# Kernel optimization log

Measured on AMD Instinct MI355X. Metric: run time of the kernel, lower is better.

The kernel has to match this reference:

```python
import jax, jax.numpy as jnp
import numpy as np

# ---- constants mirroring the torch module ----
OSAMP = 8            # temporal oversampling factor
MAX_ITER = 10        # forward solver iterations (LBFGS replaced by fixed GD)
NEG_SHIFT = 2 * OSAMP
OTP = 5              # baseline frames subtracted from ctc/aif
C_SHARP = 500.0      # sharpness constant C=500 in fermi_ir_func
LR = 0.1             # fixed step size for the deterministic forward solve


def interp_linear_1d(x, size):
    # interp_linear_1D: linear upsampling along last (time) axis
    return jax.image.resize(x, x.shape[:-1] + (size,), method='linear')


def fermi_ir(eta, t_os):
    # eta: [B,3,H,W] = (amplitude A, decay rate k, delay t0); t_os: [Tos]
    tsh = t_os - t_os[NEG_SHIFT]                    # negative time shift
    A = eta[:, 0][..., None]                        # [B,H,W,1]
    k = eta[:, 1][..., None]
    t0 = eta[:, 2][..., None]
    step = jax.nn.sigmoid(C_SHARP * tsh)            # sharp causal onset (C=500)
    return A * jax.nn.sigmoid(k * (t0 - tsh)) * step  # [B,H,W,Tos]


def convolve(aif, ir):
    # linear convolution along time via FFT; output aligned with neg_shift offset
    Tos = ir.shape[-1]
    n = 2 * Tos
    Fa = jnp.fft.rfft(aif, n=n, axis=-1)            # [B,1,1,n/2+1]
    Fi = jnp.fft.rfft(ir, n=n, axis=-1)             # [B,H,W,n/2+1]
    full = jnp.fft.irfft(Fa * Fi, n=n, axis=-1)
    return jax.lax.dynamic_slice_in_dim(full, NEG_SHIFT, Tos, axis=-1)


def make_objective(ctc, aif, time, eta_prior, lambda_reg):
    # preprocessing from FermiDataConsLBFGS.forward
    aif = aif - aif[..., :OTP].mean(-1, keepdims=True)
    ctc = ctc - ctc[..., :OTP].mean(-1, keepdims=True)
    Tos = OSAMP * ctc.shape[-1]
    aif_os = interp_linear_1d(aif, Tos)
    ctc_os = interp_linear_1d(ctc, Tos)
    t_os = interp_linear_1d(time, Tos)
    ctc_dc = ctc_os[..., ::OSAMP]                   # [B,H,W,T]
    C_nn = (eta_prior ** 2).sum(axis=(0, 2, 3), keepdims=True)  # [1,3,1,1]
    C_dc = (ctc_dc ** 2).sum()
    sp_lam = jax.nn.softplus(lambda_reg).squeeze()

    def F_obj(eta):  # FermiDConsObj.__call__ (OD disabled: indx_dc = all frames)
        ir = fermi_ir(eta, t_os)
        ctc_est = convolve(aif_os, ir)[..., ::OSAMP] / OSAMP
        dc = ((ctc_dc - ctc_est) ** 2 / C_dc).sum()
        reg = sp_lam * (((eta - eta_prior) ** 2) / C_nn).sum()
        pos = (jax.nn.relu(-eta) ** 2).sum()
        return dc + reg + pos
    return F_obj


def setup_inputs():
    key = jax.random.key(0)
    k1, k2, k3, k4 = jax.random.split(key, 4)
    B, H, W, T = 1, 128, 128, 64
    ctc = jax.random.normal(k1, (B, H, W, T), jnp.float32) * 0.1
    aif = jax.random.uniform(k2, (B, 1, 1, T), jnp.float32)
    time = jnp.arange(T, dtype=jnp.float32)
    seg = jnp.ones((B, H, W), jnp.int32)
    eta_nn = jax.random.uniform(k3, (B, 3, H, W), jnp.float32)
    lambda_reg = jax.random.normal(k4, (1,), jnp.float32)
    return {"ctc": ctc, "aif": aif, "time": time, "seg": seg,
            "eta_nn": eta_nn, "lambda_reg": lambda_reg}


def reference(ctc, aif, time, seg, eta_nn, lambda_reg):
    # seg only affects the (disabled) outlier-detection path
    F_obj = make_objective(ctc, aif, time, eta_nn, lambda_reg)
    gradF = jax.grad(F_obj)

    def step(eta, _):
        return eta - LR * gradF(eta), None

    eta_pi, _ = jax.lax.scan(step, eta_nn, None, length=MAX_ITER)
    return eta_pi
```

## Files before the change

kernel.cpp:

```cpp
#include <hip/hip_runtime.h>
#include <math.h>

#define T_IN 64
#define NPIX 16384
#define MAX_ITER 10
#define NSLOT 43
#define MAGIC 0x13579BDFu

typedef _Float16 half8_t __attribute__((ext_vector_type(8)));
typedef __fp16   fp16x2  __attribute__((ext_vector_type(2)));
typedef float    f32x4   __attribute__((ext_vector_type(4)));
typedef int      i32x4   __attribute__((ext_vector_type(4)));

union H8 { half8_t v; fp16x2 h2[4]; i32x4 i4; };

__device__ __forceinline__ float rcp_fast(float x) { return __builtin_amdgcn_rcpf(x); }

__global__ __launch_bounds__(256, 1) void k_all(
        const float* __restrict__ ctc,  const float* __restrict__ aif,
        const float* __restrict__ timev,const float* __restrict__ lam,
        const float* __restrict__ eta,  unsigned int* __restrict__ flags,
        f32x4* __restrict__ partials,   float* __restrict__ out) {
    __shared__ i32x4 Bs[NSLOT * 64];
    __shared__ float tshs[512];
    __shared__ float aifos[512];
    __shared__ float a_s[64], t_s[64];
    __shared__ f32x4 red[4];

    const int tid  = threadIdx.x;
    const int lane = tid & 63;
    const int wid  = tid >> 6;
    const int q = lane >> 4, n = lane & 15;
    const int pixbase = blockIdx.x * 64 + wid * 16;
    const int mypix   = pixbase + n;

    if (tid < 64) { a_s[tid] = aif[tid]; t_s[tid] = timev[tid]; }
    float A  = eta[mypix];
    float K  = eta[NPIX + mypix];
    float T0 = eta[2*NPIX + mypix];
    const float pA = A, pK = K, pT = T0;
    __syncthreads();
    {
        float m5a = 0.2f * (a_s[0]+a_s[1]+a_s[2]+a_s[3]+a_s[4]);
        float t16;
        {
            float xx = 1.5625f; int i0 = (int)xx; float f = xx - (float)i0;
            t16 = t_s[i0]*(1.0f-f) + t_s[i0+1]*f;
        }
        #pragma unroll
        for (int rep = 0; rep < 2; ++rep) {
            int i = tid + 256*rep;
            float x = ((float)i - 3.5f) * 0.125f;
            float ao, to;
            if (x <= 0.0f)       { ao = a_s[0]  - m5a; to = t_s[0];  }
            else if (x >= 63.0f) { ao = a_s[63] - m5a; to = t_s[63]; }
            else {
                int i0 = (int)x; float f = x - (float)i0;
                ao = (a_s[i0]-m5a)*(1.0f-f) + (a_s[i0+1]-m5a)*f;
                to = t_s[i0]*(1.0f-f) + t_s[i0+1]*f;
            }
            aifos[i] = ao;
            tshs[i]  = to - t16;
        }
    }

    float dcreg[4][4];
    #pragma unroll
    for (int reg = 0; reg < 4; ++reg) {
        const float* cp = ctc + (pixbase + q*4 + reg) * T_IN;
        float m5 = 0.2f * (cp[0]+cp[1]+cp[2]+cp[3]+cp[4]);
        #pragma unroll
        for (int nt = 0; nt < 4; ++nt) {
            int d = nt*16 + n;
            float cc = cp[d] - m5;
            float cm = cp[(d > 0) ? d-1 : 0] - m5;
            dcreg[nt][reg] = (d == 0) ? cc : (0.4375f*cm + 0.5625f*cc);
        }
    }

    {
        float vs = 0.f;
        #pragma unroll
        for (int nt = 0; nt < 4; ++nt)
            #pragma unroll
            for (int r2 = 0; r2 < 4; ++r2) vs += dcreg[nt][r2]*dcreg[nt][r2];
        f32x4 pv = (f32x4){vs, 0.25f*A*A, 0.25f*K*K, 0.25f*T0*T0};
        #pragma unroll
        for (int m = 1; m < 64; m <<= 1) {
            pv.x += __shfl_xor(pv.x, m); pv.y += __shfl_xor(pv.y, m);
            pv.z += __shfl_xor(pv.z, m); pv.w += __shfl_xor(pv.w, m);
        }
        if (lane == 0) red[wid] = pv;
    }
    __syncthreads();
    if (tid == 0) {
        f32x4 s = red[0] + red[1] + red[2] + red[3];
        partials[blockIdx.x] = s;
        __threadfence();
        __hip_atomic_store(&flags[blockIdx.x], MAGIC, __ATOMIC_RELEASE,
                           __HIP_MEMORY_SCOPE_AGENT);
    }

    for (int idx = tid; idx < NSLOT * 64; idx += 256) {
        int slot = idx >> 6, l = idx & 63;
        int kt, nt;
        if (slot < 20)      { kt = slot >> 2; nt = slot & 3; }
        else if (slot < 32) { int s = slot - 20; int d3 = s / 3; kt = 5 + d3; nt = 1 + (s - 3*d3); }
        else if (slot < 40) { int s = slot - 32; kt = 9 + (s >> 1); nt = 2 + (s & 1); }
        else                { kt = 13 + (slot - 40); nt = 3; }
        int kbase = 32*kt + 8*(l >> 4);
        int m = 16 + 8 * (16*nt + (l & 15));
        H8 bh;
        #pragma unroll
        for (int jj = 0; jj < 4; ++jj) {
            float v[2];
            #pragma unroll
            for (int h = 0; h < 2; ++h) {
                int k  = kbase + 2*jj + h;
                int ai = m - k;
                float s2 = 1.0f / (1.0f + __expf(-500.0f * tshs[k]));
                v[h] = (ai >= 0 && ai < 512) ? s2 * aifos[ai] * 0.125f : 0.0f;
            }
            bh.h2[jj] = (fp16x2){(__fp16)v[0], (__fp16)v[1]};
        }
        Bs[idx] = bh.i4;
    }
    __syncthreads();

    i32x4 Breg[NSLOT];
    #pragma unroll
    for (int s = 0; s < NSLOT; ++s) Breg[s] = Bs[s*64 + lane];

    while (__hip_atomic_load(&flags[tid], __ATOMIC_ACQUIRE,
                             __HIP_MEMORY_SCOPE_AGENT) != MAGIC)
        __builtin_amdgcn_s_sleep(2);
    __syncthreads();

    f32x4 tot = partials[lane] + partials[64+lane] + partials[128+lane]
              + partials[192+lane];
    #pragma unroll
    for (int m = 1; m < 64; m <<= 1) {
        tot.x += __shfl_xor(tot.x, m); tot.y += __shfl_xor(tot.y, m);
        tot.z += __shfl_xor(tot.z, m); tot.w += __shfl_xor(tot.w, m);
    }
    float spl;
    {
        float xl = lam[0];
        spl = (xl > 0.0f) ? (xl + log1pf(__expf(-xl))) : log1pf(__expf(xl));
    }
    const float cdc2 = 2.0f / tot.x;
    const float rgA  = 2.0f * spl / tot.y;
    const float rgK  = 2.0f * spl / tot.z;
    const float rgT  = 2.0f * spl / tot.w;

    constexpr int NTMIN[16] = {0,0,0,0,0,1,1,1,1,2,2,2,2,3,3,3};
    constexpr int TOFS[16]  = {0,4,8,12,16,20,23,26,29,32,34,36,38,40,41,42};

    #pragma unroll 1
    for (int it = 0; it < MAX_ITER; ++it) {
        f32x4 acc[3][4];
        #pragma unroll
        for (int f = 0; f < 3; ++f)
            #pragma unroll
            for (int t = 0; t < 4; ++t)
                acc[f][t] = (f32x4){0.f, 0.f, 0.f, 0.f};

        float nK = -K;
        float r  = __expf(0.125f * K);
        #pragma unroll
        for (int kt = 0; kt < 16; ++kt) {
            f32x4 tv0 = *(const f32x4*)&tshs[32*kt + 8*q];
            f32x4 tv1 = *(const f32x4*)&tshs[32*kt + 8*q + 4];
            float d1[8];
            d1[0]=T0-tv0[0]; d1[1]=T0-tv0[1]; d1[2]=T0-tv0[2]; d1[3]=T0-tv0[3];
            d1[4]=T0-tv1[0]; d1[5]=T0-tv1[1]; d1[6]=T0-tv1[2]; d1[7]=T0-tv1[3];
            float x[8];
            if (kt == 0 || kt == 15) {
                bool edge = (kt == 0) ? (q == 0) : (q == 3);
                if (edge) {
                    #pragma unroll
                    for (int j = 0; j < 8; ++j) x[j] = __expf(nK * d1[j]);
                } else {
                    x[0] = __expf(nK * d1[0]);
                    #pragma unroll
                    for (int j = 1; j < 8; ++j) x[j] = x[j-1] * r;
                }
            } else {
                x[0] = __expf(nK * d1[0]);
                #pragma unroll
                for (int j = 1; j < 8; ++j) x[j] = x[j-1] * r;
            }
            H8 F0h, F1h, F2h;
            #pragma unroll
            for (int jj = 0; jj < 4; ++jj) {
                float s1a = rcp_fast(1.0f + x[2*jj]);
                float s1b = rcp_fast(1.0f + x[2*jj+1]);
                fp16x2 sh  = (fp16x2){(__fp16)s1a, (__fp16)s1b};
                fp16x2 d1h = __builtin_amdgcn_cvt_pkrtz(d1[2*jj], d1[2*jj+1]);
                fp16x2 eh  = sh - sh*sh;
                F0h.h2[jj] = sh;
                F1h.h2[jj] = eh * d1h;
                F2h.h2[jj] = eh;
            }
            #pragma unroll
            for (int nt = NTMIN[kt]; nt < 4; ++nt) {
                int slot = TOFS[kt] + nt - NTMIN[kt];
                H8 bh; bh.i4 = Breg[slot];
                acc[0][nt] = __builtin_amdgcn_mfma_f32_16x16x32_f16(F0h.v, bh.v, acc[0][nt], 0, 0, 0);
                acc[1][nt] = __builtin_amdgcn_mfma_f32_16x16x32_f16(F1h.v, bh.v, acc[1][nt], 0, 0, 0);
                acc[2][nt] = __builtin_amdgcn_mfma_f32_16x16x32_f16(F2h.v, bh.v, acc[2][nt], 0, 0, 0);
            }
        }

        float Ap[4];
        #pragma unroll
        for (int rr2 = 0; rr2 < 4; ++rr2) Ap[rr2] = __shfl(A, q*4 + rr2);

        float SA[4], SK[4], ST[4];
        #pragma unroll
        for (int r2 = 0; r2 < 4; ++r2) { SA[r2]=0.f; SK[r2]=0.f; ST[r2]=0.f; }
        #pragma unroll
        for (int nt = 0; nt < 4; ++nt)
            #pragma unroll
            for (int r2 = 0; r2 < 4; ++r2) {
                float Y0 = acc[0][nt][r2], Y1 = acc[1][nt][r2], Y2 = acc[2][nt][r2];
                float rr = fmaf(Ap[r2], Y0, -dcreg[nt][r2]);
                SA[r2] = fmaf(rr, Y0, SA[r2]);
                SK[r2] = fmaf(rr, Y1, SK[r2]);
                ST[r2] = fmaf(rr, Y2, ST[r2]);
            }
        #pragma unroll
        for (int r2 = 0; r2 < 4; ++r2)
            #pragma unroll
            for (int m = 1; m < 16; m <<= 1) {
                SA[r2] += __shfl_xor(SA[r2], m);
                SK[r2] += __shfl_xor(SK[r2], m);
                ST[r2] += __shfl_xor(ST[r2], m);
            }
        int src = (n >> 2) * 16;
        float GA = 0.f, GK = 0.f, GT = 0.f;
        #pragma unroll
        for (int r2 = 0; r2 < 4; ++r2) {
            float tA = __shfl(SA[r2], src);
            float tK = __shfl(SK[r2], src);
            float tT = __shfl(ST[r2], src);
            if ((n & 3) == r2) { GA = tA; GK = tK; GT = tT; }
        }

        float gA = fmaf(rgA, A  - pA, cdc2 * GA)         + 2.0f * fminf(A,  0.f);
        float gK = fmaf(rgK, K  - pK, cdc2 * A * GK)     + 2.0f * fminf(K,  0.f);
        float gT = fmaf(rgT, T0 - pT, cdc2 * A * K * GT) + 2.0f * fminf(T0, 0.f);
        A  -= 0.1f * gA;
        K  -= 0.1f * gK;
        T0 -= 0.1f * gT;
    }

    if (lane < 16) {
        out[mypix]          = A;
        out[NPIX + mypix]   = K;
        out[2*NPIX + mypix] = T0;
    }
}

extern "C" void kernel_launch(void* const* d_in, const int* in_sizes, int n_in,
                              void* d_out, int out_size, void* d_ws, size_t ws_size,
                              hipStream_t stream) {
    const float* ctc   = (const float*)d_in[0];
    const float* aif   = (const float*)d_in[1];
    const float* timev = (const float*)d_in[2];
    const float* eta   = (const float*)d_in[4];
    const float* lam   = (const float*)d_in[5];
    float* out = (float*)d_out;
    f32x4*        partials = (f32x4*)d_ws;
    unsigned int* flags    = (unsigned int*)((char*)d_ws + 4096);

    k_all<<<NPIX / 64, 256, 0, stream>>>(ctc, aif, timev, lam, eta,
                                         flags, partials, out);
}
```

Before: 117.8 us.

## Split K-dimension of MFMA convolution across wave pairs per pixel group

Doubles the block to 512 threads so two waves share each 16-pixel group, each handling alternating k-tiles (even/odd) of the convolution GEMM with about half the B-fragment registers. Partial accumulators are reduced through shared memory, one wave computes the gradient step and broadcasts the updated parameters back via LDS. This aims to double MFMA/transcendental parallelism per CU and reduce register pressure, at the cost of two extra block barriers and LDS traffic per iteration.

```diff
diff --git a/kernel.cpp b/kernel.cpp
--- a/kernel.cpp
+++ b/kernel.cpp
@@ -16,12 +16,73 @@
 
 __device__ __forceinline__ float rcp_fast(float x) { return __builtin_amdgcn_rcpf(x); }
 
-__global__ __launch_bounds__(256, 1) void k_all(
+constexpr int NTMIN[16]   = {0,0,0,0,0,1,1,1,1,2,2,2,2,3,3,3};
+constexpr int KTS[2][8]   = {{0,2,4,6,8,10,12,14},{1,3,5,7,9,11,13,15}};
+constexpr int LBASE[2][8] = {{0,4,8,12,15,18,20,22},{0,4,8,11,14,16,18,19}};
+constexpr int SLOTS[2][23] = {
+  {0,1,2,3,8,9,10,11,16,17,18,19,23,24,25,29,30,31,34,35,38,39,41},
+  {4,5,6,7,12,13,14,15,20,21,22,26,27,28,32,33,36,37,40,42,0,0,0}};
+
+template<int P>
+__device__ __forceinline__ void kloop(float K, float T0, int q,
+        const float* tshs, const i32x4 (&Breg)[23], f32x4 (&acc)[3][4]) {
+    float nK = -K;
+    float r  = __expf(0.125f * K);
+    #pragma unroll
+    for (int i = 0; i < 8; ++i) {
+        const int kt = KTS[P][i];
+        f32x4 tv0 = *(const f32x4*)&tshs[32*kt + 8*q];
+        f32x4 tv1 = *(const f32x4*)&tshs[32*kt + 8*q + 4];
+        float d1[8];
+        d1[0]=T0-tv0[0]; d1[1]=T0-tv0[1]; d1[2]=T0-tv0[2]; d1[3]=T0-tv0[3];
+        d1[4]=T0-tv1[0]; d1[5]=T0-tv1[1]; d1[6]=T0-tv1[2]; d1[7]=T0-tv1[3];
+        float x[8];
+        if (kt == 0 || kt == 15) {
+            bool edge = (kt == 0) ? (q == 0) : (q == 3);
+            if (edge) {
+                #pragma unroll
+                for (int j = 0; j < 8; ++j) x[j] = __expf(nK * d1[j]);
+            } else {
+                x[0] = __expf(nK * d1[0]);
+                #pragma unroll
+                for (int j = 1; j < 8; ++j) x[j] = x[j-1] * r;
+            }
+        } else {
+            x[0] = __expf(nK * d1[0]);
+            #pragma unroll
+            for (int j = 1; j < 8; ++j) x[j] = x[j-1] * r;
+        }
+        H8 F0h, F1h, F2h;
+        #pragma unroll
+        for (int jj = 0; jj < 4; ++jj) {
+            float s1a = rcp_fast(1.0f + x[2*jj]);
+            float s1b = rcp_fast(1.0f + x[2*jj+1]);
+            fp16x2 sh  = (fp16x2){(__fp16)s1a, (__fp16)s1b};
+            fp16x2 d1h = __builtin_amdgcn_cvt_pkrtz(d1[2*jj], d1[2*jj+1]);
+            fp16x2 eh  = sh - sh*sh;
+            F0h.h2[jj] = sh;
+            F1h.h2[jj] = eh * d1h;
+            F2h.h2[jj] = eh;
+        }
+        #pragma unroll
+        for (int nt = NTMIN[kt]; nt < 4; ++nt) {
+            int sl = LBASE[P][i] + nt - NTMIN[kt];
+            H8 bh; bh.i4 = Breg[sl];
+            acc[0][nt] = __builtin_amdgcn_mfma_f32_16x16x32_f16(F0h.v, bh.v, acc[0][nt], 0, 0, 0);
+            acc[1][nt] = __builtin_amdgcn_mfma_f32_16x16x32_f16(F1h.v, bh.v, acc[1][nt], 0, 0, 0);
+            acc[2][nt] = __builtin_amdgcn_mfma_f32_16x16x32_f16(F2h.v, bh.v, acc[2][nt], 0, 0, 0);
+        }
+    }
+}
+
+__global__ __launch_bounds__(512, 2) void k_all(
         const float* __restrict__ ctc,  const float* __restrict__ aif,
         const float* __restrict__ timev,const float* __restrict__ lam,
         const float* __restrict__ eta,  unsigned int* __restrict__ flags,
         f32x4* __restrict__ partials,   float* __restrict__ out) {
     __shared__ i32x4 Bs[NSLOT * 64];
+    __shared__ f32x4 cbuf[4][64][12];
+    __shared__ float ebuf[4][16][4];
     __shared__ float tshs[512];
     __shared__ float aifos[512];
     __shared__ float a_s[64], t_s[64];
@@ -30,8 +91,10 @@
     const int tid  = threadIdx.x;
     const int lane = tid & 63;
     const int wid  = tid >> 6;
+    const int par  = wid & 1;
+    const int pair = wid >> 1;
     const int q = lane >> 4, n = lane & 15;
-    const int pixbase = blockIdx.x * 64 + wid * 16;
+    const int pixbase = blockIdx.x * 64 + pair * 16;
     const int mypix   = pixbase + n;
 
     if (tid < 64) { a_s[tid] = aif[tid]; t_s[tid] = timev[tid]; }
@@ -47,38 +110,34 @@
             float xx = 1.5625f; int i0 = (int)xx; float f = xx - (float)i0;
             t16 = t_s[i0]*(1.0f-f) + t_s[i0+1]*f;
         }
-        #pragma unroll
-        for (int rep = 0; rep < 2; ++rep) {
-            int i = tid + 256*rep;
-            float x = ((float)i - 3.5f) * 0.125f;
-            float ao, to;
-            if (x <= 0.0f)       { ao = a_s[0]  - m5a; to = t_s[0];  }
-            else if (x >= 63.0f) { ao = a_s[63] - m5a; to = t_s[63]; }
-            else {
-                int i0 = (int)x; float f = x - (float)i0;
-                ao = (a_s[i0]-m5a)*(1.0f-f) + (a_s[i0+1]-m5a)*f;
-                to = t_s[i0]*(1.0f-f) + t_s[i0+1]*f;
-            }
-            aifos[i] = ao;
-            tshs[i]  = to - t16;
-        }
+        int i = tid;
+        float x = ((float)i - 3.5f) * 0.125f;
+        float ao, to;
+        if (x <= 0.0f)       { ao = a_s[0]  - m5a; to = t_s[0];  }
+        else if (x >= 63.0f) { ao = a_s[63] - m5a; to = t_s[63]; }
+        else {
+            int i0 = (int)x; float f = x - (float)i0;
+            ao = (a_s[i0]-m5a)*(1.0f-f) + (a_s[i0+1]-m5a)*f;
+            to = t_s[i0]*(1.0f-f) + t_s[i0+1]*f;
+        }
+        aifos[i] = ao;
+        tshs[i]  = to - t16;
     }
 
     float dcreg[4][4];
-    #pragma unroll
-    for (int reg = 0; reg < 4; ++reg) {
-        const float* cp = ctc + (pixbase + q*4 + reg) * T_IN;
-        float m5 = 0.2f * (cp[0]+cp[1]+cp[2]+cp[3]+cp[4]);
-        #pragma unroll
-        for (int nt = 0; nt < 4; ++nt) {
-            int d = nt*16 + n;
-            float cc = cp[d] - m5;
-            float cm = cp[(d > 0) ? d-1 : 0] - m5;
-            dcreg[nt][reg] = (d == 0) ? cc : (0.4375f*cm + 0.5625f*cc);
-        }
-    }
-
-    {
+    if (par == 0) {
+        #pragma unroll
+        for (int reg = 0; reg < 4; ++reg) {
+            const float* cp = ctc + (pixbase + q*4 + reg) * T_IN;
+            float m5 = 0.2f * (cp[0]+cp[1]+cp[2]+cp[3]+cp[4]);
+            #pragma unroll
+            for (int nt = 0; nt < 4; ++nt) {
+                int d = nt*16 + n;
+                float cc = cp[d] - m5;
+                float cm = cp[(d > 0) ? d-1 : 0] - m5;
+                dcreg[nt][reg] = (d == 0) ? cc : (0.4375f*cm + 0.5625f*cc);
+            }
+        }
         float vs = 0.f;
         #pragma unroll
         for (int nt = 0; nt < 4; ++nt)
@@ -90,7 +149,7 @@
             pv.x += __shfl_xor(pv.x, m); pv.y += __shfl_xor(pv.y, m);
             pv.z += __shfl_xor(pv.z, m); pv.w += __shfl_xor(pv.w, m);
         }
-        if (lane == 0) red[wid] = pv;
+        if (lane == 0) red[pair] = pv;
     }
     __syncthreads();
     if (tid == 0) {
@@ -101,7 +160,7 @@
                            __HIP_MEMORY_SCOPE_AGENT);
     }
 
-    for (int idx = tid; idx < NSLOT * 64; idx += 256) {
+    for (int idx = tid; idx < NSLOT * 64; idx += 512) {
         int slot = idx >> 6, l = idx & 63;
         int kt, nt;
         if (slot < 20)      { kt = slot >> 2; nt = slot & 3; }
@@ -127,13 +186,19 @@
     }
     __syncthreads();
 
-    i32x4 Breg[NSLOT];
-    #pragma unroll
-    for (int s = 0; s < NSLOT; ++s) Breg[s] = Bs[s*64 + lane];
-
-    while (__hip_atomic_load(&flags[tid], __ATOMIC_ACQUIRE,
-                             __HIP_MEMORY_SCOPE_AGENT) != MAGIC)
-        __builtin_amdgcn_s_sleep(2);
+    i32x4 Breg[23];
+    if (par == 0) {
+        #pragma unroll
+        for (int s = 0; s < 23; ++s) Breg[s] = Bs[SLOTS[0][s]*64 + lane];
+    } else {
+        #pragma unroll
+        for (int s = 0; s < 20; ++s) Breg[s] = Bs[SLOTS[1][s]*64 + lane];
+    }
+
+    if (tid < 256)
+        while (__hip_atomic_load(&flags[tid], __ATOMIC_ACQUIRE,
+                                 __HIP_MEMORY_SCOPE_AGENT) != MAGIC)
+            __builtin_amdgcn_s_sleep(2);
     __syncthreads();
 
     f32x4 tot = partials[lane] + partials[64+lane] + partials[128+lane]
@@ -153,9 +218,6 @@
     const float rgK  = 2.0f * spl / tot.z;
     const float rgT  = 2.0f * spl / tot.w;
 
-    constexpr int NTMIN[16] = {0,0,0,0,0,1,1,1,1,2,2,2,2,3,3,3};
-    constexpr int TOFS[16]  = {0,4,8,12,16,20,23,26,29,32,34,36,38,40,41,42};
-
     #pragma unroll 1
     for (int it = 0; it < MAX_ITER; ++it) {
         f32x4 acc[3][4];
@@ -165,97 +227,83 @@
             for (int t = 0; t < 4; ++t)
                 acc[f][t] = (f32x4){0.f, 0.f, 0.f, 0.f};
 
-        float nK = -K;
-        float r  = __expf(0.125f * K);
-        #pragma unroll
-        for (int kt = 0; kt < 16; ++kt) {
-            f32x4 tv0 = *(const f32x4*)&tshs[32*kt + 8*q];
-            f32x4 tv1 = *(const f32x4*)&tshs[32*kt + 8*q + 4];
-            float d1[8];
-            d1[0]=T0-tv0[0]; d1[1]=T0-tv0[1]; d1[2]=T0-tv0[2]; d1[3]=T0-tv0[3];
-            d1[4]=T0-tv1[0]; d1[5]=T0-tv1[1]; d1[6]=T0-tv1[2]; d1[7]=T0-tv1[3];
-            float x[8];
-            if (kt == 0 || kt == 15) {
-                bool edge = (kt == 0) ? (q == 0) : (q == 3);
-                if (edge) {
-                    #pragma unroll
-                    for (int j = 0; j < 8; ++j) x[j] = __expf(nK * d1[j]);
-                } else {
-                    x[0] = __expf(nK * d1[0]);
-                    #pragma unroll
-                    for (int j = 1; j < 8; ++j) x[j] = x[j-1] * r;
+        if (par == 0) kloop<0>(K, T0, q, tshs, Breg, acc);
+        else          kloop<1>(K, T0, q, tshs, Breg, acc);
+
+        if (par == 1) {
+            #pragma unroll
+            for (int f = 0; f < 3; ++f)
+                #pragma unroll
+                for (int t = 0; t < 4; ++t)
+                    cbuf[pair][lane][f*4+t] = acc[f][t];
+        }
+        __syncthreads();
+
+        if (par == 0) {
+            #pragma unroll
+            for (int f = 0; f < 3; ++f)
+                #pragma unroll
+                for (int t = 0; t < 4; ++t)
+                    acc[f][t] += cbuf[pair][lane][f*4+t];
+
+            float Ap[4];
+            #pragma unroll
+            for (int rr2 = 0; rr2 < 4; ++rr2) Ap[rr2] = __shfl(A, q*4 + rr2);
+
+            float SA[4], SK[4], ST[4];
+            #pragma unroll
+            for (int r2 = 0; r2 < 4; ++r2) { SA[r2]=0.f; SK[r2]=0.f; ST[r2]=0.f; }
+            #pragma unroll
+            for (int nt = 0; nt < 4; ++nt)
+                #pragma unroll
+                for (int r2 = 0; r2 < 4; ++r2) {
+                    float Y0 = acc[0][nt][r2], Y1 = acc[1][nt][r2], Y2 = acc[2][nt][r2];
+                    float rr = fmaf(Ap[r2], Y0, -dcreg[nt][r2]);
+                    SA[r2] = fmaf(rr, Y0, SA[r2]);
+                    SK[r2] = fmaf(rr, Y1, SK[r2]);
+                    ST[r2] = fmaf(rr, Y2, ST[r2]);
                 }
-            } else {
-                x[0] = __expf(nK * d1[0]);
-                #pragma unroll
-                for (int j = 1; j < 8; ++j) x[j] = x[j-1] * r;
-            }
-            H8 F0h, F1h, F2h;
-            #pragma unroll
-            for (int jj = 0; jj < 4; ++jj) {
-                float s1a = rcp_fast(1.0f + x[2*jj]);
-                float s1b = rcp_fast(1.0f + x[2*jj+1]);
-                fp16x2 sh  = (fp16x2){(__fp16)s1a, (__fp16)s1b};
-                fp16x2 d1h = __builtin_amdgcn_cvt_pkrtz(d1[2*jj], d1[2*jj+1]);
-                fp16x2 eh  = sh - sh*sh;
-                F0h.h2[jj] = sh;
-                F1h.h2[jj] = eh * d1h;
-                F2h.h2[jj] = eh;
-            }
-            #pragma unroll
-            for (int nt = NTMIN[kt]; nt < 4; ++nt) {
-                int slot = TOFS[kt] + nt - NTMIN[kt];
-                H8 bh; bh.i4 = Breg[slot];
-                acc[0][nt] = __builtin_amdgcn_mfma_f32_16x16x32_f16(F0h.v, bh.v, acc[0][nt], 0, 0, 0);
-                acc[1][nt] = __builtin_amdgcn_mfma_f32_16x16x32_f16(F1h.v, bh.v, acc[1][nt], 0, 0, 0);
-                acc[2][nt] = __builtin_amdgcn_mfma_f32_16x16x32_f16(F2h.v, bh.v, acc[2][nt], 0, 0, 0);
-            }
-        }
-
-        float Ap[4];
-        #pragma unroll
-        for (int rr2 = 0; rr2 < 4; ++rr2) Ap[rr2] = __shfl(A, q*4 + rr2);
-
-        float SA[4], SK[4], ST[4];
-        #pragma unroll
-        for (int r2 = 0; r2 < 4; ++r2) { SA[r2]=0.f; SK[r2]=0.f; ST[r2]=0.f; }
-        #pragma unroll
-        for (int nt = 0; nt < 4; ++nt)
+            #pragma unroll
+            for (int r2 = 0; r2 < 4; ++r2)
+                #pragma unroll
+                for (int m = 1; m < 16; m <<= 1) {
+                    SA[r2] += __shfl_xor(SA[r2], m);
+                    SK[r2] += __shfl_xor(SK[r2], m);
+                    ST[r2] += __shfl_xor(ST[r2], m);
+                }
+            int src = (n >> 2) * 16;
+            float GA = 0.f, GK = 0.f, GT = 0.f;
             #pragma unroll
             for (int r2 = 0; r2 < 4; ++r2) {
-                float Y0 = acc[0][nt][r2], Y1 = acc[1][nt][r2], Y2 = acc[2][nt][r2];
-                float rr = fmaf(Ap[r2], Y0, -dcreg[nt][r2]);
-                SA[r2] = fmaf(rr, Y0, SA[r2]);
-                SK[r2] = fmaf(rr, Y1, SK[r2]);
-                ST[r2] = fmaf(rr, Y2, ST[r2]);
-            }
-        #pragma unroll
-        for (int r2 = 0; r2 < 4; ++r2)
-            #pragma unroll
-            for (int m = 1; m < 16; m <<= 1) {
-                SA[r2] += __shfl_xor(SA[r2], m);
-                SK[r2] += __shfl_xor(SK[r2], m);
-                ST[r2] += __shfl_xor(ST[r2], m);
-            }
-        int src = (n >> 2) * 16;
-        float GA = 0.f, GK = 0.f, GT = 0.f;
-        #pragma unroll
-        for (int r2 = 0; r2 < 4; ++r2) {
-            float tA = __shfl(SA[r2], src);
-            float tK = __shfl(SK[r2], src);
-            float tT = __shfl(ST[r2], src);
-            if ((n & 3) == r2) { GA = tA; GK = tK; GT = tT; }
-        }
-
-        float gA = fmaf(rgA, A  - pA, cdc2 * GA)         + 2.0f * fminf(A,  0.f);
-        float gK = fmaf(rgK, K  - pK, cdc2 * A * GK)     + 2.0f * fminf(K,  0.f);
-        float gT = fmaf(rgT, T0 - pT, cdc2 * A * K * GT) + 2.0f * fminf(T0, 0.f);
-        A  -= 0.1f * gA;
-        K  -= 0.1f * gK;
-        T0 -= 0.1f * gT;
-    }
-
-    if (lane < 16) {
+                float tA = __shfl(SA[r2], src);
+                float tK = __shfl(SK[r2], src);
+                float tT = __shfl(ST[r2], src);
+                if ((n & 3) == r2) { GA = tA; GK = tK; GT = tT; }
+            }
+
+            float gA = fmaf(rgA, A  - pA, cdc2 * GA)         + 2.0f * fminf(A,  0.f);
+            float gK = fmaf(rgK, K  - pK, cdc2 * A * GK)     + 2.0f * fminf(K,  0.f);
+            float gT = fmaf(rgT, T0 - pT, cdc2 * A * K * GT) + 2.0f * fminf(T0, 0.f);
+            A  -= 0.1f * gA;
+            K  -= 0.1f * gK;
+            T0 -= 0.1f * gT;
+
+            if (lane < 16) {
+                ebuf[pair][n][0] = A;
+                ebuf[pair][n][1] = K;
+                ebuf[pair][n][2] = T0;
+            }
+        }
+        __syncthreads();
+
+        if (par == 1) {
+            A  = ebuf[pair][n][0];
+            K  = ebuf[pair][n][1];
+            T0 = ebuf[pair][n][2];
+        }
+    }
+
+    if (par == 0 && lane < 16) {
         out[mypix]          = A;
         out[NPIX + mypix]   = K;
         out[2*NPIX + mypix] = T0;
@@ -274,6 +322,6 @@
     f32x4*        partials = (f32x4*)d_ws;
     unsigned int* flags    = (unsigned int*)((char*)d_ws + 4096);
 
-    k_all<<<NPIX / 64, 256, 0, stream>>>(ctc, aif, timev, lam, eta,
+    k_all<<<NPIX / 64, 512, 0, stream>>>(ctc, aif, timev, lam, eta,
                                          flags, partials, out);
 }
```

Measured after the change: 125.9 us. +6.9%, slower.
